# Kernel tuning notes

Measured on AMD Instinct MI355X. Metric: run time of the kernel, lower is better.

Reference implementation:

```python
import jax, jax.numpy as jnp
import numpy as np

B, S, D = 8, 4096, 4096
H = D // 4          # mlp router hidden
CAPACITY = 0.5      # fraction of active tokens selected per batch row
ALPHA = 1.0         # router_alpha logit scale


def setup_inputs() -> dict:
    key = jax.random.key(0)
    k_h, k_m, k_w1, k_b1, k_w2, k_b2 = jax.random.split(key, 6)
    hidden_states = jax.random.normal(k_h, (B, S, D), dtype=jnp.float32)
    active_mask = jax.random.randint(k_m, (B, S), 0, 2).astype(jnp.bool_)
    W1 = jax.random.normal(k_w1, (D, H), dtype=jnp.float32) / np.sqrt(D)
    b1 = jax.random.normal(k_b1, (H,), dtype=jnp.float32) * 0.01
    W2 = jax.random.normal(k_w2, (H, 1), dtype=jnp.float32) / np.sqrt(H)
    b2 = jax.random.normal(k_b2, (1,), dtype=jnp.float32) * 0.01
    return {"hidden_states": hidden_states, "active_mask": active_mask,
            "W1": W1, "b1": b1, "W2": W2, "b2": b2}


def reference(hidden_states, active_mask, W1, b1, W2, b2):
    # MLP router: Linear(D, D//4) -> GELU(exact) -> Linear(D//4, 1), squeeze
    h = jax.nn.gelu(jnp.einsum('bsd,dh->bsh', hidden_states, W1) + b1,
                    approximate=False)                      # [B,S,H]
    router_logits = jnp.einsum('bsh,ho->bso', h, W2)[..., 0] + b2[0]  # [B,S]
    router_scores = jax.nn.sigmoid(router_logits * ALPHA)   # [B,S]

    # mask inactive tokens with -inf for selection
    masked_scores = jnp.where(active_mask, router_scores, -jnp.inf)
    num_active = active_mask.sum(axis=-1).astype(jnp.int32)  # [B]

    # per-row variable k: k = floor(capacity * num_active), clamped to [1, num_active]
    k = jnp.floor(CAPACITY * num_active.astype(jnp.float32)).astype(jnp.int32)
    k = jnp.clip(k, 1, jnp.maximum(num_active, 1))
    k = jnp.where(num_active == 0, 0, k)                     # [B]

    # vectorized variable-k top-k via ranks: rank r of each token in its row
    order = jnp.argsort(-masked_scores, axis=-1)             # [B,S], descending
    ranks = jnp.zeros((B, S), dtype=jnp.int32).at[
        jnp.arange(B)[:, None], order].set(
        jnp.broadcast_to(jnp.arange(S, dtype=jnp.int32), (B, S)))
    selected_mask = ranks < k[:, None]                       # [B,S] bool

    router_weights = router_scores * selected_mask.astype(router_scores.dtype)
    return router_weights, selected_mask
```

## Files before the change

kernel.cpp:

```cpp
#include <hip/hip_runtime.h>
#include <math.h>

typedef unsigned int u32;
typedef unsigned short u16;
typedef __attribute__((ext_vector_type(8))) short short8;
typedef __attribute__((ext_vector_type(4))) float f32x4;

constexpr int BB = 8;
constexpr int S  = 4096;
constexpr int D  = 4096;
constexpr int H  = 1024;
constexpr int M  = BB * S;
constexpr int BM = 128;
constexpr int BN = 256;
constexpr int BK = 32;
constexpr int NTB    = H / BN;
constexpr int MTILES = M / BM;
constexpr int KSTEPS = D / BK;
constexpr int CHUNK  = 4 * BN * 8;


__device__ inline void split_bf16(float x, u16& h, u16& l) {
    u32 u  = __float_as_uint(x);
    u32 hu = u & 0xFFFF0000u;
    h = (u16)(u >> 16);
    float r = x - __uint_as_float(hu);
    l = (u16)(__float_as_uint(r) >> 16);
}

__device__ inline f32x4 mfma16(short8 a, short8 b, f32x4 c) {
    return __builtin_amdgcn_mfma_f32_16x16x32_bf16(a, b, c, 0, 0, 0);
}

__device__ inline void gl_lds16(const u16* g, u16* l) {
    __builtin_amdgcn_global_load_lds(
        (const __attribute__((address_space(1))) u32*)g,
        (__attribute__((address_space(3))) u32*)l, 16, 0, 0);
}

__global__ __launch_bounds__(1024) void pack_w1(
    const float* __restrict__ W1, u16* __restrict__ bh, u16* __restrict__ bl)
{
    int blk = blockIdx.x;
    int ntb = blk >> 7, ks = blk & 127;
    int t  = threadIdx.x;
    int k8 = t >> 8, n = t & 255;
    int kbase = ks * 32 + k8 * 8;

    short8 vh, vl;
    #pragma unroll
    for (int j = 0; j < 8; ++j) {
        float x = W1[(size_t)(kbase + j) * H + ntb * 256 + n];
        u16 hh, ll;
        split_bf16(x, hh, ll);
        vh[j] = (short)hh;
        vl[j] = (short)ll;
    }
    size_t base = (size_t)blk * CHUNK + k8 * 2048 + n * 8;
    *reinterpret_cast<short8*>(bh + base) = vh;
    *reinterpret_cast<short8*>(bl + base) = vl;
}

struct Areg { f32x4 a0lo, a0hi, a1lo, a1hi; };

__device__ inline void loadA(const float* p0, const float* p1, int k, Areg& r) {
    const float* q0 = p0 + k * BK;
    const float* q1 = p1 + k * BK;
    r.a0lo = *(const f32x4*)(q0);
    r.a0hi = *(const f32x4*)(q0 + 4);
    r.a1lo = *(const f32x4*)(q1);
    r.a1hi = *(const f32x4*)(q1 + 4);
}

__global__ __launch_bounds__(256, 2) void gemm_mfma(
    const float* __restrict__ X,
    const u16*   __restrict__ Bph, const u16* __restrict__ Bpl,
    const float* __restrict__ b1,  const float* __restrict__ W2,
    float*       __restrict__ part)
{
    __shared__ u16 Bh[2][CHUNK];
    __shared__ u16 Bl[2][CHUNK];

    int b   = blockIdx.x;
    int xcd = b & 7;
    int j   = b >> 3;
    int ntb = j & 3;
    int mtg = j >> 2;
    int mt  = mtg * 8 + xcd;
    int m0  = mt * BM;
    int n0  = ntb * BN;

    int tid  = threadIdx.x;
    int lane = tid & 63, wv = tid >> 6;
    int li   = lane & 15, quad = lane >> 4;

    const float* aptr0 = X + (size_t)(m0 + wv * 32 + li) * D + quad * 8;
    const float* aptr1 = aptr0 + (size_t)16 * D;

    const u16* gsrc = (wv < 2) ? Bph : Bpl;
    int soff = (wv & 1) * 4096;
    u16* l0 = ((wv < 2) ? Bh[0] : Bl[0]) + soff;
    u16* l1 = ((wv < 2) ? Bh[1] : Bl[1]) + soff;
    const u16* gb = gsrc + soff;

    f32x4 acc[2][16] = {};
    Areg rA, rB;

    auto stage = [&](u16* ldst, int k) {
        const u16* g = gb + (size_t)(ntb * 128 + k) * CHUNK + lane * 8;
        #pragma unroll
        for (int r = 0; r < 8; ++r)
            gl_lds16(g + r * 512, ldst + r * 512 + lane * 8);
    };

    auto computeStep = [&](const Areg& ar, const u16* BhBuf, const u16* BlBuf) {
        short8 ah[2], al[2];
        #pragma unroll
        for (int e = 0; e < 4; ++e) {
            u16 h, l;
            split_bf16(ar.a0lo[e], h, l); ah[0][e]     = (short)h; al[0][e]     = (short)l;
            split_bf16(ar.a0hi[e], h, l); ah[0][e + 4] = (short)h; al[0][e + 4] = (short)l;
            split_bf16(ar.a1lo[e], h, l); ah[1][e]     = (short)h; al[1][e]     = (short)l;
            split_bf16(ar.a1hi[e], h, l); ah[1][e + 4] = (short)h; al[1][e + 4] = (short)l;
        }
        #pragma unroll
        for (int ntl = 0; ntl < 16; ++ntl) {
            int off = quad * 2048 + (ntl * 16 + li) * 8;
            short8 bhf = *reinterpret_cast<const short8*>(BhBuf + off);
            short8 blf = *reinterpret_cast<const short8*>(BlBuf + off);
            #pragma unroll
            for (int mtl = 0; mtl < 2; ++mtl) {
                acc[mtl][ntl] = mfma16(ah[mtl], bhf, acc[mtl][ntl]);
                acc[mtl][ntl] = mfma16(al[mtl], bhf, acc[mtl][ntl]);
                acc[mtl][ntl] = mfma16(ah[mtl], blf, acc[mtl][ntl]);
            }
        }
    };

    stage(l0, 0);
    loadA(aptr0, aptr1, 0, rA);
    __syncthreads();

    for (int ks = 0; ks < KSTEPS; ks += 2) {
        int k1 = ks + 1;
        int k2 = (ks + 2 < KSTEPS) ? ks + 2 : KSTEPS - 1;

        stage(l1, k1);
        loadA(aptr0, aptr1, k1, rB);
        computeStep(rA, Bh[1 - 1], Bl[0]);
        __syncthreads();

        stage(l0, k2);
        loadA(aptr0, aptr1, k2, rA);
        computeStep(rB, Bh[1], Bl[1]);
        __syncthreads();
    }

    float b1v[16], w2v[16];
    #pragma unroll
    for (int ntl = 0; ntl < 16; ++ntl) {
        b1v[ntl] = b1[n0 + ntl * 16 + li];
        w2v[ntl] = W2[n0 + ntl * 16 + li];
    }
    #pragma unroll
    for (int mtl = 0; mtl < 2; ++mtl) {
        #pragma unroll
        for (int r = 0; r < 4; ++r) {
            float s = 0.f;
            #pragma unroll
            for (int ntl = 0; ntl < 16; ++ntl) {
                float x = acc[mtl][ntl][r] + b1v[ntl];
                float g = 0.5f * x * (1.0f + erff(x * 0.70710678118654752f));
                s += g * w2v[ntl];
            }
            s += __shfl_xor(s, 1, 64);
            s += __shfl_xor(s, 2, 64);
            s += __shfl_xor(s, 4, 64);
            s += __shfl_xor(s, 8, 64);
            if (li == 0) {
                int row = m0 + wv * 32 + mtl * 16 + quad * 4 + r;
                part[(size_t)ntb * M + row] = s;
            }
        }
    }
}

__global__ __launch_bounds__(256) void select_topk(
    const float* __restrict__ part,
    const int*   __restrict__ mask,
    const float* __restrict__ b2,
    float*       __restrict__ out)
{
    __shared__ unsigned us[S];
    __shared__ int      na_s, cnt_s, cgt_s, cge_s;
    __shared__ unsigned lo_s, hi_s;

    int brow = blockIdx.x;
    int tid  = threadIdx.x;

    if (tid == 0) na_s = 0;
    __syncthreads();

    float b2v = b2[0];
    int local_na = 0;
    for (int s = tid; s < S; s += 256) {
        float sum = 0.f;
        #pragma unroll
        for (int t = 0; t < NTB; ++t) sum += part[t * M + brow * S + s];
        float logit = sum + b2v;
        float sc = 1.0f / (1.0f + expf(-logit));
        int a = mask[brow * S + s];
        us[s] = a ? __float_as_uint(sc) : 0u;
        local_na += (a ? 1 : 0);
    }
    atomicAdd(&na_s, local_na);
    __syncthreads();

    int n_act = na_s;
    int k = (n_act >= 1) ? max(n_act >> 1, 1) : 0;

    unsigned T = 0;
    if (k > 0) {
        if (tid == 0) { lo_s = 1u; hi_s = 0x3F800000u; }
        __syncthreads();
        while (true) {
            unsigned lo = lo_s, hi = hi_s;
            if (lo >= hi) break;
            unsigned mid = lo + ((hi - lo + 1u) >> 1);
            int local = 0;
            for (int s = tid; s < S; s += 256) local += (us[s] >= mid) ? 1 : 0;
            if (tid == 0) cnt_s = 0;
            __syncthreads();
            #pragma unroll
            for (int off = 32; off > 0; off >>= 1)
                local += __shfl_down(local, off, 64);
            if ((tid & 63) == 0) atomicAdd(&cnt_s, local);
            __syncthreads();
            int c = cnt_s;
            if (tid == 0) { if (c >= k) lo_s = mid; else hi_s = mid - 1u; }
            __syncthreads();
        }
        T = lo_s;

        int lgt = 0, lge = 0;
        for (int s = tid; s < S; s += 256) {
            lgt += (us[s] > T) ? 1 : 0;
            lge += (us[s] >= T) ? 1 : 0;
        }
        if (tid == 0) { cgt_s = 0; cge_s = 0; }
        __syncthreads();
        #pragma unroll
        for (int off = 32; off > 0; off >>= 1) {
            lgt += __shfl_down(lgt, off, 64);
            lge += __shfl_down(lge, off, 64);
        }
        if ((tid & 63) == 0) { atomicAdd(&cgt_s, lgt); atomicAdd(&cge_s, lge); }
        __syncthreads();
        int c_gt = cgt_s, c_ge = cge_s;
        int need_eq = k - c_gt;
        if (c_ge - c_gt != need_eq) {
            if (tid == 0) {
                int taken = 0;
                for (int s = 0; s < S; ++s) {
                    if (us[s] == T) {
                        if (taken >= need_eq) us[s] = 0u;
                        ++taken;
                    }
                }
            }
            __syncthreads();
        }
    }
    __syncthreads();

    for (int s = tid; s < S; s += 256) {
        bool sel = (k > 0) && (us[s] >= T);
        float sc = __uint_as_float(us[s]);
        out[brow * S + s]     = sel ? sc : 0.0f;
        out[M + brow * S + s] = sel ? 1.0f : 0.0f;
    }
}

extern "C" void kernel_launch(void* const* d_in, const int* in_sizes, int n_in,
                              void* d_out, int out_size, void* d_ws, size_t ws_size,
                              hipStream_t stream)
{
    const float* X    = (const float*)d_in[0];
    const int*   mask = (const int*)  d_in[1];
    const float* W1   = (const float*)d_in[2];
    const float* b1   = (const float*)d_in[3];
    const float* W2   = (const float*)d_in[4];
    const float* b2   = (const float*)d_in[5];
    float* out  = (float*)d_out;

    float* part = (float*)d_ws;
    u16*   Bph  = (u16*)((char*)d_ws + (2u  << 20));
    u16*   Bpl  = (u16*)((char*)d_ws + (10u << 20));

    hipLaunchKernelGGL(pack_w1,   dim3(NTB * KSTEPS),  dim3(1024), 0, stream, W1, Bph, Bpl);
    hipLaunchKernelGGL(gemm_mfma, dim3(MTILES * NTB),  dim3(256),  0, stream,
                       X, Bph, Bpl, b1, W2, part);
    hipLaunchKernelGGL(select_topk, dim3(BB), dim3(256), 0, stream, part, mask, b2, out);
}
```

Before: 1.300 ms.

## Switch GEMM to 32x32x16 MFMA with 2x2 wave tiling

Replaces 16x16x32 bf16 MFMAs with 32x32x16 MFMAs and arranges the four waves as a 2x2 grid over M and N. Each wave now reads fewer B fragments from LDS per k-step, and the A split into bf16 hi/lo moves to after the barrier. The epilogue reduction adapts to the 32-wide layout and writes twice as many partial slabs, which the selection kernel then sums. The cost is duplicated A global loads across waves and a larger partial buffer.

```diff
diff --git a/kernel.cpp b/kernel.cpp
--- a/kernel.cpp
+++ b/kernel.cpp
@@ -5,6 +5,7 @@
 typedef unsigned short u16;
 typedef __attribute__((ext_vector_type(8))) short short8;
 typedef __attribute__((ext_vector_type(4))) float f32x4;
+typedef __attribute__((ext_vector_type(16))) float f32x16;
 
 constexpr int BB = 8;
 constexpr int S  = 4096;
@@ -15,6 +16,7 @@
 constexpr int BN = 256;
 constexpr int BK = 32;
 constexpr int NTB    = H / BN;
+constexpr int NSLAB  = NTB * 2;
 constexpr int MTILES = M / BM;
 constexpr int KSTEPS = D / BK;
 constexpr int CHUNK  = 4 * BN * 8;
@@ -28,8 +30,8 @@
     l = (u16)(__float_as_uint(r) >> 16);
 }
 
-__device__ inline f32x4 mfma16(short8 a, short8 b, f32x4 c) {
-    return __builtin_amdgcn_mfma_f32_16x16x32_bf16(a, b, c, 0, 0, 0);
+__device__ inline f32x16 mfma32(short8 a, short8 b, f32x16 c) {
+    return __builtin_amdgcn_mfma_f32_32x32x16_bf16(a, b, c, 0, 0, 0);
 }
 
 __device__ inline void gl_lds16(const u16* g, u16* l) {
@@ -61,17 +63,6 @@
     *reinterpret_cast<short8*>(bl + base) = vl;
 }
 
-struct Areg { f32x4 a0lo, a0hi, a1lo, a1hi; };
-
-__device__ inline void loadA(const float* p0, const float* p1, int k, Areg& r) {
-    const float* q0 = p0 + k * BK;
-    const float* q1 = p1 + k * BK;
-    r.a0lo = *(const f32x4*)(q0);
-    r.a0hi = *(const f32x4*)(q0 + 4);
-    r.a1lo = *(const f32x4*)(q1);
-    r.a1hi = *(const f32x4*)(q1 + 4);
-}
-
 __global__ __launch_bounds__(256, 2) void gemm_mfma(
     const float* __restrict__ X,
     const u16*   __restrict__ Bph, const u16* __restrict__ Bpl,
@@ -92,10 +83,10 @@
 
     int tid  = threadIdx.x;
     int lane = tid & 63, wv = tid >> 6;
-    int li   = lane & 15, quad = lane >> 4;
-
-    const float* aptr0 = X + (size_t)(m0 + wv * 32 + li) * D + quad * 8;
-    const float* aptr1 = aptr0 + (size_t)16 * D;
+    int wvm  = wv >> 1,  wvn = wv & 1;
+    int l31  = lane & 31, khi = lane >> 5;
+
+    const float* aptr = X + (size_t)(m0 + wvm * 64 + l31) * D + khi * 8;
 
     const u16* gsrc = (wv < 2) ? Bph : Bpl;
     int soff = (wv & 1) * 4096;
@@ -103,8 +94,9 @@
     u16* l1 = ((wv < 2) ? Bh[1] : Bl[1]) + soff;
     const u16* gb = gsrc + soff;
 
-    f32x4 acc[2][16] = {};
-    Areg rA, rB;
+    f32x16 acc[2][4] = {};
+    f32x4  fst[2][2][2];
+    short8 ah[2][2], al[2][2];
 
     auto stage = [&](u16* ldst, int k) {
         const u16* g = gb + (size_t)(ntb * 128 + k) * CHUNK + lane * 8;
@@ -113,62 +105,86 @@
             gl_lds16(g + r * 512, ldst + r * 512 + lane * 8);
     };
 
-    auto computeStep = [&](const Areg& ar, const u16* BhBuf, const u16* BlBuf) {
-        short8 ah[2], al[2];
+    auto loadA = [&](int k) {
+        #pragma unroll
+        for (int mtl = 0; mtl < 2; ++mtl)
+        #pragma unroll
+        for (int ks2 = 0; ks2 < 2; ++ks2) {
+            const float* p = aptr + (size_t)mtl * 32 * D + k * BK + ks2 * 16;
+            fst[mtl][ks2][0] = *(const f32x4*)(p);
+            fst[mtl][ks2][1] = *(const f32x4*)(p + 4);
+        }
+    };
+
+    auto splitA = [&]() {
+        #pragma unroll
+        for (int mtl = 0; mtl < 2; ++mtl)
+        #pragma unroll
+        for (int ks2 = 0; ks2 < 2; ++ks2)
         #pragma unroll
         for (int e = 0; e < 4; ++e) {
             u16 h, l;
-            split_bf16(ar.a0lo[e], h, l); ah[0][e]     = (short)h; al[0][e]     = (short)l;
-            split_bf16(ar.a0hi[e], h, l); ah[0][e + 4] = (short)h; al[0][e + 4] = (short)l;
-            split_bf16(ar.a1lo[e], h, l); ah[1][e]     = (short)h; al[1][e]     = (short)l;
-            split_bf16(ar.a1hi[e], h, l); ah[1][e + 4] = (short)h; al[1][e + 4] = (short)l;
-        }
-        #pragma unroll
-        for (int ntl = 0; ntl < 16; ++ntl) {
-            int off = quad * 2048 + (ntl * 16 + li) * 8;
+            split_bf16(fst[mtl][ks2][0][e], h, l);
+            ah[mtl][ks2][e]     = (short)h; al[mtl][ks2][e]     = (short)l;
+            split_bf16(fst[mtl][ks2][1][e], h, l);
+            ah[mtl][ks2][e + 4] = (short)h; al[mtl][ks2][e + 4] = (short)l;
+        }
+    };
+
+    auto compute = [&](const u16* BhBuf, const u16* BlBuf) {
+        #pragma unroll
+        for (int ks2 = 0; ks2 < 2; ++ks2)
+        #pragma unroll
+        for (int ntl = 0; ntl < 4; ++ntl) {
+            int off = ((ks2 * 2 + khi) * 256 + wvn * 128 + ntl * 32 + l31) * 8;
             short8 bhf = *reinterpret_cast<const short8*>(BhBuf + off);
             short8 blf = *reinterpret_cast<const short8*>(BlBuf + off);
             #pragma unroll
             for (int mtl = 0; mtl < 2; ++mtl) {
-                acc[mtl][ntl] = mfma16(ah[mtl], bhf, acc[mtl][ntl]);
-                acc[mtl][ntl] = mfma16(al[mtl], bhf, acc[mtl][ntl]);
-                acc[mtl][ntl] = mfma16(ah[mtl], blf, acc[mtl][ntl]);
+                acc[mtl][ntl] = mfma32(ah[mtl][ks2], bhf, acc[mtl][ntl]);
+                acc[mtl][ntl] = mfma32(al[mtl][ks2], bhf, acc[mtl][ntl]);
+                acc[mtl][ntl] = mfma32(ah[mtl][ks2], blf, acc[mtl][ntl]);
             }
         }
     };
 
     stage(l0, 0);
-    loadA(aptr0, aptr1, 0, rA);
+    loadA(0);
     __syncthreads();
+    splitA();
 
     for (int ks = 0; ks < KSTEPS; ks += 2) {
         int k1 = ks + 1;
         int k2 = (ks + 2 < KSTEPS) ? ks + 2 : KSTEPS - 1;
 
         stage(l1, k1);
-        loadA(aptr0, aptr1, k1, rB);
-        computeStep(rA, Bh[1 - 1], Bl[0]);
-        __syncthreads();
+        loadA(k1);
+        compute(Bh[0], Bl[0]);
+        __syncthreads();
+        splitA();
 
         stage(l0, k2);
-        loadA(aptr0, aptr1, k2, rA);
-        computeStep(rB, Bh[1], Bl[1]);
-        __syncthreads();
-    }
-
-    float b1v[16], w2v[16];
+        loadA(k2);
+        compute(Bh[1], Bl[1]);
+        __syncthreads();
+        splitA();
+    }
+
+    float b1v[4], w2v[4];
     #pragma unroll
-    for (int ntl = 0; ntl < 16; ++ntl) {
-        b1v[ntl] = b1[n0 + ntl * 16 + li];
-        w2v[ntl] = W2[n0 + ntl * 16 + li];
-    }
+    for (int ntl = 0; ntl < 4; ++ntl) {
+        int col = n0 + wvn * 128 + ntl * 32 + l31;
+        b1v[ntl] = b1[col];
+        w2v[ntl] = W2[col];
+    }
+    int pslab = ntb * 2 + wvn;
     #pragma unroll
     for (int mtl = 0; mtl < 2; ++mtl) {
         #pragma unroll
-        for (int r = 0; r < 4; ++r) {
+        for (int r = 0; r < 16; ++r) {
             float s = 0.f;
             #pragma unroll
-            for (int ntl = 0; ntl < 16; ++ntl) {
+            for (int ntl = 0; ntl < 4; ++ntl) {
                 float x = acc[mtl][ntl][r] + b1v[ntl];
                 float g = 0.5f * x * (1.0f + erff(x * 0.70710678118654752f));
                 s += g * w2v[ntl];
@@ -177,9 +193,10 @@
             s += __shfl_xor(s, 2, 64);
             s += __shfl_xor(s, 4, 64);
             s += __shfl_xor(s, 8, 64);
-            if (li == 0) {
-                int row = m0 + wv * 32 + mtl * 16 + quad * 4 + r;
-                part[(size_t)ntb * M + row] = s;
+            s += __shfl_xor(s, 16, 64);
+            if (l31 == 0) {
+                int row = m0 + wvm * 64 + mtl * 32 + (r & 3) + 8 * (r >> 2) + 4 * khi;
+                part[(size_t)pslab * M + row] = s;
             }
         }
     }
@@ -206,7 +223,7 @@
     for (int s = tid; s < S; s += 256) {
         float sum = 0.f;
         #pragma unroll
-        for (int t = 0; t < NTB; ++t) sum += part[t * M + brow * S + s];
+        for (int t = 0; t < NSLAB; ++t) sum += part[t * M + brow * S + s];
         float logit = sum + b2v;
         float sc = 1.0f / (1.0f + expf(-logit));
         int a = mask[brow * S + s];
```

Result: slower. 1.448 ms (+11.4%).
